# Optimization experiments

Hardware: AMD Instinct MI355X
Metric: run time of the kernel (lower is better)

## Reference

```python
import jax, jax.numpy as jnp
import numpy as np
import math

D = 384; N = 1024; BATCH = 8
D_STATE = 64; D_CONV = 4; EXPAND = 2
D_INNER = EXPAND * D
DT_RANK = math.ceil(D / 16)
W_WIN = 4; N_HEADS = 4; HEAD_DIM = D // N_HEADS
BOTTLENECK = max(8, D // 4)

def _perms(n):
    side = int(math.isqrt(n))
    p0 = np.arange(n)
    p1 = np.arange(n).reshape(side, side).T.reshape(-1)   # column-major
    p2 = p0[::-1].copy()                                   # reverse horizontal
    p3 = p1[::-1].copy()                                   # reverse vertical
    return [jnp.asarray(p) for p in (p0, p1, p2, p3)]

PERMS = _perms(N)

def layernorm(x, w, b, eps=1e-5):
    mu = jnp.mean(x, -1, keepdims=True)
    var = jnp.var(x, -1, keepdims=True)
    return (x - mu) * jax.lax.rsqrt(var + eps) * w + b

def mamba(x, in_proj_w, conv_w, conv_b, x_proj_w, dt_proj_w, dt_proj_b, A_log, D_skip, out_proj_w):
    # canonical pure-python Mamba block (selective scan SSM)
    B, L, _ = x.shape
    xz = x @ in_proj_w.T                      # [B,L,2*di]
    xin, z = jnp.split(xz, 2, axis=-1)
    xc = jnp.swapaxes(xin, 1, 2)              # [B,di,L]
    xc = jax.lax.conv_general_dilated(xc, conv_w, (1,), [(D_CONV - 1, 0)], feature_group_count=D_INNER)
    u = jax.nn.silu(jnp.swapaxes(xc + conv_b[None, :, None], 1, 2))  # [B,L,di]
    x_dbl = u @ x_proj_w.T                    # [B,L,dt_rank+2*ds]
    dt, Bm, Cm = jnp.split(x_dbl, [DT_RANK, DT_RANK + D_STATE], axis=-1)
    dt = jax.nn.softplus(dt @ dt_proj_w.T + dt_proj_b)  # [B,L,di]
    A = -jnp.exp(A_log)                       # [di,ds]
    def step(h, inp):
        dt_t, B_t, C_t, u_t = inp             # [B,di],[B,ds],[B,ds],[B,di]
        dA = jnp.exp(dt_t[:, :, None] * A[None])
        h = dA * h + dt_t[:, :, None] * B_t[:, None, :] * u_t[:, :, None]
        y = jnp.einsum('bds,bs->bd', h, C_t)
        return h, y
    h0 = jnp.zeros((B, D_INNER, D_STATE), x.dtype)
    xs = (jnp.swapaxes(dt, 0, 1), jnp.swapaxes(Bm, 0, 1), jnp.swapaxes(Cm, 0, 1), jnp.swapaxes(u, 0, 1))
    _, ys = jax.lax.scan(step, h0, xs)
    y = jnp.swapaxes(ys, 0, 1) + u * D_skip
    return (y * jax.nn.silu(z)) @ out_proj_w.T

def local_attn(x, qkv_w, qkv_b, ao_w, ao_b):
    # sliding-window MHA over windows of W_WIN tokens (N % W_WIN == 0 here, no pad)
    B, Nn, Dd = x.shape
    xw = x.reshape(B * (Nn // W_WIN), W_WIN, Dd)
    qkv = xw @ qkv_w.T + qkv_b
    q, k, v = jnp.split(qkv, 3, axis=-1)
    def heads(t):
        return t.reshape(t.shape[0], W_WIN, N_HEADS, HEAD_DIM).transpose(0, 2, 1, 3)
    q, k, v = heads(q), heads(k), heads(v)
    scores = jnp.einsum('bhqd,bhkd->bhqk', q, k) / math.sqrt(HEAD_DIM)
    attn = jax.nn.softmax(scores, axis=-1)
    o = jnp.einsum('bhqk,bhkd->bhqd', attn, v).transpose(0, 2, 1, 3).reshape(-1, W_WIN, Dd)
    return (o @ ao_w.T + ao_b).reshape(B, Nn, Dd)

def setup_inputs() -> dict:
    key = jax.random.key(0)
    ks = jax.random.split(key, 16)
    def rn(k, shape, scale=0.02):
        return jax.random.normal(k, shape, jnp.float32) * scale
    return dict(
        x=jax.random.normal(ks[0], (BATCH, N, D), jnp.float32),
        r_w1=rn(ks[1], (BOTTLENECK, D)), r_b1=jnp.zeros((BOTTLENECK,), jnp.float32),
        r_w2=rn(ks[2], (4, BOTTLENECK)), r_b2=jnp.zeros((4,), jnp.float32),
        ln1_w=jnp.ones((D,), jnp.float32), ln1_b=jnp.zeros((D,), jnp.float32),
        ln2_w=jnp.ones((D,), jnp.float32), ln2_b=jnp.zeros((D,), jnp.float32),
        in_proj_w=rn(ks[3], (2 * D_INNER, D)),
        conv_w=rn(ks[4], (D_INNER, 1, D_CONV), 0.1), conv_b=jnp.zeros((D_INNER,), jnp.float32),
        x_proj_w=rn(ks[5], (DT_RANK + 2 * D_STATE, D_INNER)),
        dt_proj_w=rn(ks[6], (D_INNER, DT_RANK), 0.1),
        dt_proj_b=jnp.full((D_INNER,), -3.0, jnp.float32) + rn(ks[7], (D_INNER,), 0.1),
        A_log=jnp.log(jnp.tile(jnp.arange(1, D_STATE + 1, dtype=jnp.float32), (D_INNER, 1))),
        D_skip=jnp.ones((D_INNER,), jnp.float32),
        out_proj_w=rn(ks[8], (D, D_INNER)),
        qkv_w=rn(ks[9], (3 * D, D)), qkv_b=jnp.zeros((3 * D,), jnp.float32),
        ao_w=rn(ks[10], (D, D)), ao_b=jnp.zeros((D,), jnp.float32),
        gate=jnp.full((1,), 0.1, jnp.float32),
        lng_w=jnp.ones((D,), jnp.float32), lng_b=jnp.zeros((D,), jnp.float32),
    )

def reference(x, r_w1, r_b1, r_w2, r_b2, ln1_w, ln1_b, ln2_w, ln2_b,
              in_proj_w, conv_w, conv_b, x_proj_w, dt_proj_w, dt_proj_b,
              A_log, D_skip, out_proj_w, qkv_w, qkv_b, ao_w, ao_b,
              gate, lng_w, lng_b):
    # ScanRouter: mean-pool -> MLP -> softmax over 4 directions (dropout=eval)
    g = jnp.mean(x, axis=1)
    h = jax.nn.gelu(g @ r_w1.T + r_b1, approximate=False)
    w = jax.nn.softmax(h @ r_w2.T + r_b2, axis=-1)   # [B,4]
    xn = layernorm(x, ln1_w, ln1_b)
    fused = jnp.zeros_like(x)
    for d in range(4):
        out = mamba(xn[:, PERMS[d], :], in_proj_w, conv_w, conv_b, x_proj_w,
                    dt_proj_w, dt_proj_b, A_log, D_skip, out_proj_w)
        fused = fused + w[:, d, None, None] * out
    x = x + fused                                    # residual (dropout=eval)
    xn2 = layernorm(x, ln2_w, ln2_b)
    ao = local_attn(xn2, qkv_w, qkv_b, ao_w, ao_b)
    return layernorm(xn2 + gate * ao, lng_w, lng_b)
```

## Files before the change

### kernel.cpp

```cpp
#include <hip/hip_runtime.h>
#include <math.h>


#define NSEQ  1024
#define DMODEL 384
#define DINNER 768
#define DSTATE 64
#define XW 152
#define SCHUNK 128

typedef unsigned short u16;
typedef __attribute__((ext_vector_type(8))) short short8;
typedef __attribute__((ext_vector_type(4))) float f32x4;

__device__ __forceinline__ float bf2f(u16 u){
  union { unsigned int i; float f; } c; c.i = ((unsigned int)u) << 16; return c.f;
}
__device__ __forceinline__ u16 f2bf(float f){
  union { float f; unsigned int i; } c; c.f = f;
  unsigned int x = c.i;
  return (u16)((x + 0x7fffu + ((x >> 16) & 1u)) >> 16);
}
__device__ __forceinline__ float4 unp4(uint2 u){
  float4 f;
  f.x = bf2f((u16)(u.x & 0xffffu)); f.y = bf2f((u16)(u.x >> 16));
  f.z = bf2f((u16)(u.y & 0xffffu)); f.w = bf2f((u16)(u.y >> 16));
  return f;
}

template<int DIR>
__device__ __forceinline__ int permi(int i){
  if (DIR == 0) return i;
  if (DIR == 1) return ((i & 31) << 5) | (i >> 5);
  if (DIR == 2) return 1023 - i;
  int j = 1023 - i; return ((j & 31) << 5) | (j >> 5);
}
template<int DIR>
__device__ __forceinline__ int znext(int zi){
  if (DIR == 0) return zi + 4;
  if (DIR == 2) return zi - 4;
  if (DIR == 1) { int t = zi + 128; return (t >= 1024) ? t - 1023 : t; }
  int t = zi - 128; return (t < 0) ? t + 1023 : t;
}

__global__ __launch_bounds__(384) void router_mean_kernel(const float* __restrict__ X, float* __restrict__ G){
  int b = blockIdx.y, chunk = blockIdx.x, c = threadIdx.x;
  float s = 0.f;
  const float* xp = X + ((size_t)b*NSEQ + (size_t)chunk*64)*DMODEL + c;
  for (int l = 0; l < 64; ++l) s += xp[(size_t)l*DMODEL];
  atomicAdd(&G[b*DMODEL + c], s * (1.f/1024.f));
}

__global__ __launch_bounds__(96) void router_mlp_kernel(const float* __restrict__ G,
    const float* __restrict__ w1, const float* __restrict__ b1,
    const float* __restrict__ w2, const float* __restrict__ b2, float* __restrict__ WR){
  int b = blockIdx.x, j = threadIdx.x;
  __shared__ float hs[96];
  __shared__ float ls[4];
  float a = b1[j];
  const float* g = G + b*DMODEL;
  for (int c = 0; c < DMODEL; ++c) a += g[c] * w1[j*DMODEL + c];
  hs[j] = 0.5f * a * (1.f + erff(a * 0.70710678118654752f));
  __syncthreads();
  if (j < 4) {
    float lg = b2[j];
    for (int jj = 0; jj < 96; ++jj) lg += hs[jj] * w2[j*96 + jj];
    ls[j] = lg;
  }
  __syncthreads();
  if (j == 0) {
    float mx = fmaxf(fmaxf(ls[0],ls[1]),fmaxf(ls[2],ls[3]));
    float e0=__expf(ls[0]-mx), e1=__expf(ls[1]-mx), e2=__expf(ls[2]-mx), e3=__expf(ls[3]-mx);
    float s = e0+e1+e2+e3;
    WR[b*4+0]=e0/s; WR[b*4+1]=e1/s; WR[b*4+2]=e2/s; WR[b*4+3]=e3/s;
  }
}

__global__ __launch_bounds__(256) void ln_bf16out_kernel(const float* __restrict__ X,
    const float* __restrict__ w, const float* __restrict__ bb, u16* __restrict__ O){
  int row = blockIdx.x*4 + (threadIdx.x >> 6);
  int lane = threadIdx.x & 63;
  const float* xr = X + (size_t)row*DMODEL;
  float v[6]; float s=0.f, s2=0.f;
  #pragma unroll
  for (int j=0;j<6;++j){ float t = xr[lane + j*64]; v[j]=t; s+=t; s2+=t*t; }
  #pragma unroll
  for (int m=1;m<64;m<<=1){ s += __shfl_xor(s,m,64); s2 += __shfl_xor(s2,m,64); }
  float mu = s*(1.f/DMODEL);
  float rs = rsqrtf(s2*(1.f/DMODEL) - mu*mu + 1e-5f);
  u16* o = O + (size_t)row*DMODEL;
  #pragma unroll
  for (int j=0;j<6;++j){ int i = lane+j*64; o[i] = f2bf((v[j]-mu)*rs*w[i] + bb[i]); }
}

__global__ __launch_bounds__(256) void ln_dual_kernel(const float* __restrict__ X,
    const float* __restrict__ w, const float* __restrict__ bb,
    float* __restrict__ O, u16* __restrict__ OB){
  int row = blockIdx.x*4 + (threadIdx.x >> 6);
  int lane = threadIdx.x & 63;
  const float* xr = X + (size_t)row*DMODEL;
  float v[6]; float s=0.f, s2=0.f;
  #pragma unroll
  for (int j=0;j<6;++j){ float t = xr[lane + j*64]; v[j]=t; s+=t; s2+=t*t; }
  #pragma unroll
  for (int m=1;m<64;m<<=1){ s += __shfl_xor(s,m,64); s2 += __shfl_xor(s2,m,64); }
  float mu = s*(1.f/DMODEL);
  float rs = rsqrtf(s2*(1.f/DMODEL) - mu*mu + 1e-5f);
  float* o = O + (size_t)row*DMODEL;
  u16* ob = OB + (size_t)row*DMODEL;
  #pragma unroll
  for (int j=0;j<6;++j){ int i = lane+j*64; float r = (v[j]-mu)*rs*w[i] + bb[i]; o[i] = r; ob[i] = f2bf(r); }
}

__global__ __launch_bounds__(256) void ln_final_kernel(const float* __restrict__ XN2,
    const float* __restrict__ AO, const float* __restrict__ gatep,
    const float* __restrict__ w, const float* __restrict__ bb, float* __restrict__ OUT){
  int row = blockIdx.x*4 + (threadIdx.x >> 6);
  int lane = threadIdx.x & 63;
  float gate = gatep[0];
  const float* xr = XN2 + (size_t)row*DMODEL;
  const float* ar = AO + (size_t)row*DMODEL;
  float v[6]; float s=0.f, s2=0.f;
  #pragma unroll
  for (int j=0;j<6;++j){ int i = lane+j*64; float t = xr[i] + gate*ar[i]; v[j]=t; s+=t; s2+=t*t; }
  #pragma unroll
  for (int m=1;m<64;m<<=1){ s += __shfl_xor(s,m,64); s2 += __shfl_xor(s2,m,64); }
  float mu = s*(1.f/DMODEL);
  float rs = rsqrtf(s2*(1.f/DMODEL) - mu*mu + 1e-5f);
  float* o = OUT + (size_t)row*DMODEL;
  #pragma unroll
  for (int j=0;j<6;++j){ int i = lane+j*64; o[i] = (v[j]-mu)*rs*w[i] + bb[i]; }
}

__global__ __launch_bounds__(256) void cvt4_kernel(const float* __restrict__ src,
    u16* __restrict__ dst, int n4){
  int i = blockIdx.x*256 + threadIdx.x;
  if (i >= n4) return;
  float4 v = ((const float4*)src)[i];
  ushort4 o; o.x=f2bf(v.x); o.y=f2bf(v.y); o.z=f2bf(v.z); o.w=f2bf(v.w);
  ((ushort4*)dst)[i] = o;
}

__global__ __launch_bounds__(256) void mgemm_kernel(
    const u16* __restrict__ A, int lda,
    const u16* __restrict__ W, int K, int N,
    const float* __restrict__ bias,
    const float* __restrict__ resid,
    int act,
    int obf,
    void* __restrict__ C, int ldc)
{
  const int lane = threadIdx.x & 63;
  const int wv = threadIdx.x >> 6;
  const int m0 = (blockIdx.y*4 + wv) * 64;
  const int n0 = blockIdx.x * 64;
  const int r  = lane & 15;
  const int kg = lane >> 4;
  f32x4 acc[4][4];
  #pragma unroll
  for (int i=0;i<4;++i){
    #pragma unroll
    for (int j=0;j<4;++j) acc[i][j] = (f32x4)0.f;
  }
  for (int k0 = 0; k0 < K; k0 += 32) {
    const bool kval = (k0 + kg*8) < K;
    short8 a[4], b[4];
    #pragma unroll
    for (int i = 0; i < 4; ++i) {
      a[i] = kval ? *(const short8*)(A + (size_t)(m0 + i*16 + r)*lda + k0 + kg*8) : (short8)0;
      int n = n0 + i*16 + r;
      b[i] = (kval && n < N) ? *(const short8*)(W + (size_t)n*K + k0 + kg*8) : (short8)0;
    }
    #pragma unroll
    for (int ai = 0; ai < 4; ++ai)
      #pragma unroll
      for (int bi = 0; bi < 4; ++bi)
        acc[ai][bi] = __builtin_amdgcn_mfma_f32_16x16x32_bf16(a[ai], b[bi], acc[ai][bi], 0, 0, 0);
  }
  #pragma unroll
  for (int ai = 0; ai < 4; ++ai) {
    int mrow = m0 + ai*16 + kg*4;
    #pragma unroll
    for (int bi = 0; bi < 4; ++bi) {
      int n = n0 + bi*16 + r;
      if (n < N) {
        #pragma unroll
        for (int q = 0; q < 4; ++q) {
          float v = acc[ai][bi][q];
          int m = mrow + q;
          if (bias) v += bias[n];
          if (act == 1) v = (v > 20.f) ? v : log1pf(__expf(v));
          if (resid) v += resid[(size_t)m*ldc + n];
          if (obf) ((u16*)C)[(size_t)m*ldc + n] = f2bf(v);
          else     ((float*)C)[(size_t)m*ldc + n] = v;
        }
      }
    }
  }
}

__global__ __launch_bounds__(256) void zsilu_kernel(u16* __restrict__ XZ){
  int idx = blockIdx.x*256 + threadIdx.x;
  int row = idx / 96, q = idx % 96;
  u16* p = XZ + (size_t)row*1536 + DINNER + q*8;
  uint4 v = *(uint4*)p;
  unsigned w0=v.x, w1=v.y, w2=v.z, w3=v.w;
  #define ZS(w) { \
    float lo = bf2f((u16)((w) & 0xffffu)); \
    float hi = bf2f((u16)((w) >> 16)); \
    lo = lo / (1.f + __expf(-lo)); \
    hi = hi / (1.f + __expf(-hi)); \
    (w) = (unsigned)f2bf(lo) | ((unsigned)f2bf(hi) << 16); }
  ZS(w0) ZS(w1) ZS(w2) ZS(w3)
  #undef ZS
  v.x=w0; v.y=w1; v.z=w2; v.w=w3;
  *(uint4*)p = v;
}

template<int DIR>
__device__ __forceinline__ float conv_acc(const u16* __restrict__ XZ,
    const float* __restrict__ cw, int b, int i, int c, float acc){
  #pragma unroll
  for (int k = 0; k < 4; ++k) {
    int ii = i - 3 + k;
    if (ii >= 0)
      acc += cw[c*4 + k] * bf2f(XZ[((size_t)b*NSEQ + permi<DIR>(ii))*1536 + c]);
  }
  return acc;
}

__global__ __launch_bounds__(256) void conv_silu_all_kernel(const u16* __restrict__ XZ,
    const float* __restrict__ cw, const float* __restrict__ cb,
    u16* __restrict__ UD4, int BS){
  int dir = blockIdx.y;
  int idx = blockIdx.x*256 + threadIdx.x;
  int c = idx % DINNER;
  int rest = idx / DINNER;
  int i = rest & 1023;
  int b = rest >> 10;
  float acc = cb[c];
  switch (dir) {
    case 0: acc = conv_acc<0>(XZ, cw, b, i, c, acc); break;
    case 1: acc = conv_acc<1>(XZ, cw, b, i, c, acc); break;
    case 2: acc = conv_acc<2>(XZ, cw, b, i, c, acc); break;
    default: acc = conv_acc<3>(XZ, cw, b, i, c, acc); break;
  }
  UD4[((size_t)(dir*BS + b)*NSEQ + i)*1536 + c] = f2bf(acc / (1.f + __expf(-acc)));
}

template<int CTRL>
__device__ __forceinline__ float dpp_add(float v){
  int t = __builtin_amdgcn_update_dpp(0, __float_as_int(v), CTRL, 0xf, 0xf, true);
  return v + __int_as_float(t);
}
__device__ __forceinline__ float row16_sum(float p){
  p = dpp_add<0x128>(p);
  p = dpp_add<0x124>(p);
  p = dpp_add<0x122>(p);
  p = dpp_add<0x121>(p);
  return p;
}

template<int DIR>
__device__ __forceinline__ void scan_body(
    const u16* __restrict__ xd, const u16* __restrict__ ud,
    const u16* __restrict__ zb,
    u16* __restrict__ ob,
    float* __restrict__ lacc,
    const float* __restrict__ A_log, const float* __restrict__ Dskip,
    float wgt, int c0w, int grp)
{
  const int lane = threadIdx.x & 63;
  const int g = lane >> 4;
  const int q = lane & 15;
  const int c = c0w + g;
  const float4 Alq = *(const float4*)(A_log + (size_t)c*DSTATE + q*4);
  const float As0 = -__expf(Alq.x), As1 = -__expf(Alq.y);
  const float As2 = -__expf(Alq.z), As3 = -__expf(Alq.w);
  const float dsk = Dskip[c];
  const u16* zp = zb + DINNER + c;
  float* lw = lacc + DIR*SCHUNK*8 + grp*4 + g;

  const u16* px0 = xd + 0*XW + 24 + q*4;
  const u16* px1 = xd + 1*XW + 24 + q*4;
  const u16* px2 = xd + 2*XW + 24 + q*4;
  const u16* px3 = xd + 3*XW + 24 + q*4;
  const u16* pu0 = ud + 0*1536 + c;
  const u16* pu1 = ud + 1*1536 + c;
  const u16* pu2 = ud + 2*1536 + c;
  const u16* pu3 = ud + 3*1536 + c;
  int zi0 = permi<DIR>(0), zi1 = permi<DIR>(1), zi2 = permi<DIR>(2), zi3 = permi<DIR>(3);

#define SLOAD(k) {                                                          \
    uint2 bd = *(const uint2*)px##k;                                        \
    uint2 cd = *(const uint2*)(px##k + 64);                                 \
    B##k = unp4(bd); C##k = unp4(cd);                                       \
    u##k = bf2f(pu##k[0]); t##k = bf2f(pu##k[768]);                         \
    z##k = bf2f(zp[(ptrdiff_t)zi##k * 1536]);                               \
    px##k += 4*XW; pu##k += 4*1536; zi##k = znext<DIR>(zi##k); }

#define SSTEP(k, l) {                                                       \
    float dtu = t##k * u##k;                                                \
    float e0 = __expf(t##k*As0), e1 = __expf(t##k*As1);                     \
    float e2 = __expf(t##k*As2), e3 = __expf(t##k*As3);                     \
    h0 = e0*h0 + dtu*B##k.x; h1 = e1*h1 + dtu*B##k.y;                       \
    h2 = e2*h2 + dtu*B##k.z; h3 = e3*h3 + dtu*B##k.w;                       \
    float p = h0*C##k.x + h1*C##k.y + h2*C##k.z + h3*C##k.w;                \
    p = row16_sum(p);                                                       \
    float o = wgt*(p + u##k*dsk)*z##k;                                      \
    if (q == 0) lw[((l)&(SCHUNK-1))*8] = o; }

  float4 B0,C0,B1,C1,B2,C2,B3,C3;
  float t0,u0,z0, t1,u1,z1, t2,u2,z2, t3,u3,z3;
  float h0=0.f, h1=0.f, h2=0.f, h3=0.f;
  SLOAD(0) SLOAD(1) SLOAD(2) SLOAD(3)
  __builtin_amdgcn_sched_barrier(0);
  for (int l0 = 0; l0 < NSEQ; l0 += SCHUNK) {
    for (int l = l0; l < l0 + SCHUNK; l += 4) {
      SSTEP(0,l)   SLOAD(0) __builtin_amdgcn_sched_barrier(0);
      SSTEP(1,l+1) SLOAD(1) __builtin_amdgcn_sched_barrier(0);
      SSTEP(2,l+2) SLOAD(2) __builtin_amdgcn_sched_barrier(0);
      SSTEP(3,l+3) SLOAD(3) __builtin_amdgcn_sched_barrier(0);
    }
    __syncthreads();
    for (int i = threadIdx.x; i < SCHUNK*8; i += 512) {
      float s = lacc[i] + lacc[SCHUNK*8 + i] + lacc[2*SCHUNK*8 + i] + lacc[3*SCHUNK*8 + i];
      int row = i >> 3, cc = i & 7;
      ob[(size_t)(l0 + row)*DINNER + cc] = f2bf(s);
    }
    __syncthreads();
  }
#undef SLOAD
#undef SSTEP
}

__global__ __launch_bounds__(512) void scan_all_kernel(
    const u16* __restrict__ XD4, const u16* __restrict__ UD4,
    const u16* __restrict__ XZ, u16* __restrict__ OB,
    const float* __restrict__ A_log, const float* __restrict__ Dskip,
    const float* __restrict__ WR, int b0, int BS)
{
  __shared__ float lacc[4*SCHUNK*8];
  const int bx = blockIdx.x;
  const int sx = (bx & 7)*12 + (bx >> 3);
  const int c0 = sx * 8;
  const int b = blockIdx.y;
  const int w = threadIdx.x >> 6;
  const int dir = w & 3;
  const int grp = w >> 2;
  const int c0w = c0 + grp*4;
  const size_t drb = ((size_t)dir*BS + b) * NSEQ;
  const u16* xd = XD4 + drb*XW;
  const u16* ud = UD4 + drb*1536;
  const u16* zz = XZ  + (size_t)b*NSEQ*1536;
  u16* ob = OB + (size_t)b*NSEQ*DINNER + c0;
  const float wgt = WR[(b0+b)*4 + dir];
  switch (dir) {
    case 0: scan_body<0>(xd, ud, zz, ob, lacc, A_log, Dskip, wgt, c0w, grp); break;
    case 1: scan_body<1>(xd, ud, zz, ob, lacc, A_log, Dskip, wgt, c0w, grp); break;
    case 2: scan_body<2>(xd, ud, zz, ob, lacc, A_log, Dskip, wgt, c0w, grp); break;
    default: scan_body<3>(xd, ud, zz, ob, lacc, A_log, Dskip, wgt, c0w, grp); break;
  }
}

__global__ __launch_bounds__(256) void attn_kernel(const float* __restrict__ QKV, u16* __restrict__ O){
  int idx = blockIdx.x*256 + threadIdx.x;
  int tq = idx & 3, h = (idx >> 2) & 3, w = idx >> 4;
  size_t row0 = (size_t)w * 4;
  const float4* qp = (const float4*)(QKV + (row0 + tq)*1152 + h*96);
  float sc[4];
  #pragma unroll
  for (int tk = 0; tk < 4; ++tk) {
    const float4* kp = (const float4*)(QKV + (row0 + tk)*1152 + 384 + h*96);
    float d = 0.f;
    #pragma unroll
    for (int j = 0; j < 24; ++j) {
      float4 qf = qp[j], kf = kp[j];
      d += qf.x*kf.x + qf.y*kf.y + qf.z*kf.z + qf.w*kf.w;
    }
    sc[tk] = d * 0.10206207261596575f;
  }
  float mx = fmaxf(fmaxf(sc[0],sc[1]),fmaxf(sc[2],sc[3]));
  float s = 0.f;
  #pragma unroll
  for (int tk=0;tk<4;++tk){ sc[tk]=__expf(sc[tk]-mx); s+=sc[tk]; }
  float inv = 1.f/s;
  #pragma unroll
  for (int tk=0;tk<4;++tk) sc[tk]*=inv;
  u16* op = O + (row0 + tq)*DMODEL + h*96;
  #pragma unroll 4
  for (int j = 0; j < 24; ++j) {
    float4 o = {0.f,0.f,0.f,0.f};
    #pragma unroll
    for (int tk=0;tk<4;++tk){
      const float4* vp = (const float4*)(QKV + (row0+tk)*1152 + 768 + h*96);
      float4 vf = vp[j];
      o.x += sc[tk]*vf.x; o.y += sc[tk]*vf.y; o.z += sc[tk]*vf.z; o.w += sc[tk]*vf.w;
    }
    ushort4 ov; ov.x=f2bf(o.x); ov.y=f2bf(o.y); ov.z=f2bf(o.z); ov.w=f2bf(o.w);
    *(ushort4*)(op + j*4) = ov;
  }
}

extern "C" void kernel_launch(void* const* d_in, const int* in_sizes, int n_in,
                              void* d_out, int out_size, void* d_ws, size_t ws_size,
                              hipStream_t stream)
{
  (void)in_sizes; (void)n_in; (void)out_size;
  const float* x         = (const float*)d_in[0];
  const float* r_w1      = (const float*)d_in[1];
  const float* r_b1      = (const float*)d_in[2];
  const float* r_w2      = (const float*)d_in[3];
  const float* r_b2      = (const float*)d_in[4];
  const float* ln1_w     = (const float*)d_in[5];
  const float* ln1_b     = (const float*)d_in[6];
  const float* ln2_w     = (const float*)d_in[7];
  const float* ln2_b     = (const float*)d_in[8];
  const float* in_proj_w = (const float*)d_in[9];
  const float* conv_w    = (const float*)d_in[10];
  const float* conv_b    = (const float*)d_in[11];
  const float* x_proj_w  = (const float*)d_in[12];
  const float* dt_proj_w = (const float*)d_in[13];
  const float* dt_proj_b = (const float*)d_in[14];
  const float* A_log     = (const float*)d_in[15];
  const float* D_skip    = (const float*)d_in[16];
  const float* out_proj_w= (const float*)d_in[17];
  const float* qkv_w     = (const float*)d_in[18];
  const float* qkv_b     = (const float*)d_in[19];
  const float* ao_w      = (const float*)d_in[20];
  const float* ao_b      = (const float*)d_in[21];
  const float* gate      = (const float*)d_in[22];
  const float* lng_w     = (const float*)d_in[23];
  const float* lng_b     = (const float*)d_in[24];

  float* ws = (float*)d_ws;
  float* WR = ws;
  float* G  = ws + 64;
  u16*  WBF = (u16*)(ws + 3200);
  u16* ipw = WBF + 0;
  u16* xpw = WBF + 589824;
  u16* dtw = WBF + 706560;
  u16* opw = WBF + 724992;
  u16* qkw = WBF + 1019904;
  u16* aow = WBF + 1462272;

  int BS = 8;
  while (BS > 1) {
    size_t need = ((size_t)808064 + (size_t)BS*1024*5296) * sizeof(float);
    if (need <= ws_size) break;
    BS >>= 1;
  }
  const int R = BS * 1024;

  (void)hipMemsetAsync(ws, 0, 4096*sizeof(float), stream);
  router_mean_kernel<<<dim3(16,8),384,0,stream>>>(x, G);
  router_mlp_kernel<<<8,96,0,stream>>>(G, r_w1, r_b1, r_w2, r_b2, WR);

  cvt4_kernel<<<576,256,0,stream>>>(in_proj_w, ipw, 147456);
  cvt4_kernel<<<114,256,0,stream>>>(x_proj_w,  xpw, 29184);
  cvt4_kernel<<<18,256,0,stream>>>(dt_proj_w,  dtw, 4608);
  cvt4_kernel<<<288,256,0,stream>>>(out_proj_w,opw, 73728);
  cvt4_kernel<<<432,256,0,stream>>>(qkv_w,     qkw, 110592);
  cvt4_kernel<<<144,256,0,stream>>>(ao_w,      aow, 36864);

  float* base = ws + 808064;
  u16*   ABF  = (u16*)base;
  u16*   XZbf = (u16*)(base + (size_t)R*384);
  u16*   UD4  = (u16*)(base + (size_t)R*1152);
  u16*   XD4  = (u16*)(base + (size_t)R*4224);
  float* XN2  = base + (size_t)R*4528;
  float* AOb  = base + (size_t)R*4912;
  float* X2   = (float*)UD4;
  float* QKV  = (float*)UD4 + (size_t)R*384;
  u16*   ATTO = (u16*)((float*)UD4 + (size_t)R*1536);

  for (int s = 0; s < 8/BS; ++s) {
    const int b0 = s * BS;
    const size_t xoff = (size_t)b0 * NSEQ * DMODEL;

    ln_bf16out_kernel<<<R/4,256,0,stream>>>(x + xoff, ln1_w, ln1_b, ABF);
    mgemm_kernel<<<dim3(24,R/256),256,0,stream>>>(ABF,384, ipw,384,1536, nullptr,nullptr,0,1, XZbf,1536);
    zsilu_kernel<<<(R*96)/256,256,0,stream>>>(XZbf);
    conv_silu_all_kernel<<<dim3(3*R,4),256,0,stream>>>(XZbf, conv_w, conv_b, UD4, BS);
    mgemm_kernel<<<dim3(3,R/64),256,0,stream>>>(UD4,1536, xpw,768,152, nullptr,nullptr,0,1, XD4,152);
    mgemm_kernel<<<dim3(12,R/64),256,0,stream>>>(XD4,152, dtw,24,768, dt_proj_b,nullptr,1,1, UD4+768,1536);
    scan_all_kernel<<<dim3(96,BS),512,0,stream>>>(XD4, UD4, XZbf, ABF, A_log, D_skip, WR, b0, BS);
    mgemm_kernel<<<dim3(6,R/256),256,0,stream>>>(ABF,768, opw,768,384, nullptr,x + xoff,0,0, X2,384);
    ln_dual_kernel<<<R/4,256,0,stream>>>(X2, ln2_w, ln2_b, XN2, ABF);
    mgemm_kernel<<<dim3(18,R/256),256,0,stream>>>(ABF,384, qkw,384,1152, qkv_b,nullptr,0,0, QKV,1152);
    attn_kernel<<<R/64,256,0,stream>>>(QKV, ATTO);
    mgemm_kernel<<<dim3(6,R/256),256,0,stream>>>(ATTO,384, aow,384,384, ao_b,nullptr,0,0, AOb,384);
    ln_final_kernel<<<R/4,256,0,stream>>>(XN2, AOb, gate, lng_w, lng_b, (float*)d_out + xoff);
  }
}
```

Baseline: 1.089 ms.

## Fuse z-SiLU into in_proj GEMM, fp32 x_proj output, scalar dt_proj, exp2 scan

Folds the SiLU on the z half into the in_proj GEMM epilogue and drops the separate zsilu pass. x_proj now writes fp32 instead of bf16. The dt projection becomes a plain scalar kernel that reads the fp32 x_proj output and the fp32 weights, replacing a MFMA GEMM with K=24. The scan uses raw v_exp_f32 with log2e folded into A, loads B/C as float4, and buffers four outputs so it issues one vector LDS store, using a transposed lacc layout. This trades more memory traffic for the fp32 intermediate and a scalar dt_proj against fewer launches and cheaper scan instructions.

```diff
diff --git a/kernel.cpp b/kernel.cpp
--- a/kernel.cpp
+++ b/kernel.cpp
@@ -21,11 +21,10 @@
   unsigned int x = c.i;
   return (u16)((x + 0x7fffu + ((x >> 16) & 1u)) >> 16);
 }
-__device__ __forceinline__ float4 unp4(uint2 u){
-  float4 f;
-  f.x = bf2f((u16)(u.x & 0xffffu)); f.y = bf2f((u16)(u.x >> 16));
-  f.z = bf2f((u16)(u.y & 0xffffu)); f.w = bf2f((u16)(u.y >> 16));
-  return f;
+__device__ __forceinline__ float exp2raw(float x){
+  float r;
+  asm("v_exp_f32 %0, %1" : "=v"(r) : "v"(x));
+  return r;
 }
 
 template<int DIR>
@@ -146,8 +145,7 @@
     const u16* __restrict__ W, int K, int N,
     const float* __restrict__ bias,
     const float* __restrict__ resid,
-    int act,
-    int obf,
+    int act, int obf,
     void* __restrict__ C, int ldc)
 {
   const int lane = threadIdx.x & 63;
@@ -190,6 +188,7 @@
           int m = mrow + q;
           if (bias) v += bias[n];
           if (act == 1) v = (v > 20.f) ? v : log1pf(__expf(v));
+          if (act == 2 && n >= DINNER) v = v / (1.f + __expf(-v));
           if (resid) v += resid[(size_t)m*ldc + n];
           if (obf) ((u16*)C)[(size_t)m*ldc + n] = f2bf(v);
           else     ((float*)C)[(size_t)m*ldc + n] = v;
@@ -199,22 +198,18 @@
   }
 }
 
-__global__ __launch_bounds__(256) void zsilu_kernel(u16* __restrict__ XZ){
+__global__ __launch_bounds__(256) void dtproj_kernel(const float* __restrict__ XDf,
+    const float* __restrict__ w, const float* __restrict__ b, u16* __restrict__ DT){
   int idx = blockIdx.x*256 + threadIdx.x;
-  int row = idx / 96, q = idx % 96;
-  u16* p = XZ + (size_t)row*1536 + DINNER + q*8;
-  uint4 v = *(uint4*)p;
-  unsigned w0=v.x, w1=v.y, w2=v.z, w3=v.w;
-  #define ZS(w) { \
-    float lo = bf2f((u16)((w) & 0xffffu)); \
-    float hi = bf2f((u16)((w) >> 16)); \
-    lo = lo / (1.f + __expf(-lo)); \
-    hi = hi / (1.f + __expf(-hi)); \
-    (w) = (unsigned)f2bf(lo) | ((unsigned)f2bf(hi) << 16); }
-  ZS(w0) ZS(w1) ZS(w2) ZS(w3)
-  #undef ZS
-  v.x=w0; v.y=w1; v.z=w2; v.w=w3;
-  *(uint4*)p = v;
+  int c = idx % DINNER;
+  int row = idx / DINNER;
+  const float* xr = XDf + (size_t)row*XW;
+  const float* wr = w + c*24;
+  float a = b[c];
+  #pragma unroll
+  for (int k = 0; k < 24; ++k) a += xr[k]*wr[k];
+  a = (a > 20.f) ? a : log1pf(__expf(a));
+  DT[(size_t)row*1536 + c] = f2bf(a);
 }
 
 template<int DIR>
@@ -263,7 +258,7 @@
 
 template<int DIR>
 __device__ __forceinline__ void scan_body(
-    const u16* __restrict__ xd, const u16* __restrict__ ud,
+    const float* __restrict__ xdf, const u16* __restrict__ ud,
     const u16* __restrict__ zb,
     u16* __restrict__ ob,
     float* __restrict__ lacc,
@@ -274,17 +269,18 @@
   const int g = lane >> 4;
   const int q = lane & 15;
   const int c = c0w + g;
+  const float L2E = 1.4426950408889634f;
   const float4 Alq = *(const float4*)(A_log + (size_t)c*DSTATE + q*4);
-  const float As0 = -__expf(Alq.x), As1 = -__expf(Alq.y);
-  const float As2 = -__expf(Alq.z), As3 = -__expf(Alq.w);
+  const float As0 = -__expf(Alq.x)*L2E, As1 = -__expf(Alq.y)*L2E;
+  const float As2 = -__expf(Alq.z)*L2E, As3 = -__expf(Alq.w)*L2E;
   const float dsk = Dskip[c];
   const u16* zp = zb + DINNER + c;
-  float* lw = lacc + DIR*SCHUNK*8 + grp*4 + g;
-
-  const u16* px0 = xd + 0*XW + 24 + q*4;
-  const u16* px1 = xd + 1*XW + 24 + q*4;
-  const u16* px2 = xd + 2*XW + 24 + q*4;
-  const u16* px3 = xd + 3*XW + 24 + q*4;
+  float* lw = lacc + DIR*(8*SCHUNK) + (grp*4 + g)*SCHUNK;
+
+  const float* px0 = xdf + 0*XW + 24 + q*4;
+  const float* px1 = xdf + 1*XW + 24 + q*4;
+  const float* px2 = xdf + 2*XW + 24 + q*4;
+  const float* px3 = xdf + 3*XW + 24 + q*4;
   const u16* pu0 = ud + 0*1536 + c;
   const u16* pu1 = ud + 1*1536 + c;
   const u16* pu2 = ud + 2*1536 + c;
@@ -292,23 +288,21 @@
   int zi0 = permi<DIR>(0), zi1 = permi<DIR>(1), zi2 = permi<DIR>(2), zi3 = permi<DIR>(3);
 
 #define SLOAD(k) {                                                          \
-    uint2 bd = *(const uint2*)px##k;                                        \
-    uint2 cd = *(const uint2*)(px##k + 64);                                 \
-    B##k = unp4(bd); C##k = unp4(cd);                                       \
+    B##k = *(const float4*)px##k;                                           \
+    C##k = *(const float4*)(px##k + 64);                                    \
     u##k = bf2f(pu##k[0]); t##k = bf2f(pu##k[768]);                         \
     z##k = bf2f(zp[(ptrdiff_t)zi##k * 1536]);                               \
     px##k += 4*XW; pu##k += 4*1536; zi##k = znext<DIR>(zi##k); }
 
-#define SSTEP(k, l) {                                                       \
+#define SSTEP(k, ov_) {                                                     \
     float dtu = t##k * u##k;                                                \
-    float e0 = __expf(t##k*As0), e1 = __expf(t##k*As1);                     \
-    float e2 = __expf(t##k*As2), e3 = __expf(t##k*As3);                     \
+    float e0 = exp2raw(t##k*As0), e1 = exp2raw(t##k*As1);                   \
+    float e2 = exp2raw(t##k*As2), e3 = exp2raw(t##k*As3);                   \
     h0 = e0*h0 + dtu*B##k.x; h1 = e1*h1 + dtu*B##k.y;                       \
     h2 = e2*h2 + dtu*B##k.z; h3 = e3*h3 + dtu*B##k.w;                       \
     float p = h0*C##k.x + h1*C##k.y + h2*C##k.z + h3*C##k.w;                \
     p = row16_sum(p);                                                       \
-    float o = wgt*(p + u##k*dsk)*z##k;                                      \
-    if (q == 0) lw[((l)&(SCHUNK-1))*8] = o; }
+    ov_ = wgt*(p + u##k*dsk)*z##k; }
 
   float4 B0,C0,B1,C1,B2,C2,B3,C3;
   float t0,u0,z0, t1,u1,z1, t2,u2,z2, t3,u3,z3;
@@ -317,15 +311,22 @@
   __builtin_amdgcn_sched_barrier(0);
   for (int l0 = 0; l0 < NSEQ; l0 += SCHUNK) {
     for (int l = l0; l < l0 + SCHUNK; l += 4) {
-      SSTEP(0,l)   SLOAD(0) __builtin_amdgcn_sched_barrier(0);
-      SSTEP(1,l+1) SLOAD(1) __builtin_amdgcn_sched_barrier(0);
-      SSTEP(2,l+2) SLOAD(2) __builtin_amdgcn_sched_barrier(0);
-      SSTEP(3,l+3) SLOAD(3) __builtin_amdgcn_sched_barrier(0);
+      float o0,o1,o2,o3;
+      SSTEP(0,o0) SLOAD(0) __builtin_amdgcn_sched_barrier(0);
+      SSTEP(1,o1) SLOAD(1) __builtin_amdgcn_sched_barrier(0);
+      SSTEP(2,o2) SLOAD(2) __builtin_amdgcn_sched_barrier(0);
+      SSTEP(3,o3) SLOAD(3)
+      if (q == 0) {
+        float4 ov = {o0,o1,o2,o3};
+        *(float4*)(lw + (l & (SCHUNK-1))) = ov;
+      }
+      __builtin_amdgcn_sched_barrier(0);
     }
     __syncthreads();
-    for (int i = threadIdx.x; i < SCHUNK*8; i += 512) {
-      float s = lacc[i] + lacc[SCHUNK*8 + i] + lacc[2*SCHUNK*8 + i] + lacc[3*SCHUNK*8 + i];
-      int row = i >> 3, cc = i & 7;
+    for (int i = threadIdx.x; i < 8*SCHUNK; i += 512) {
+      int cc = i & 7, row = i >> 3;
+      int li = cc*SCHUNK + row;
+      float s = lacc[li] + lacc[8*SCHUNK + li] + lacc[16*SCHUNK + li] + lacc[24*SCHUNK + li];
       ob[(size_t)(l0 + row)*DINNER + cc] = f2bf(s);
     }
     __syncthreads();
@@ -335,12 +336,12 @@
 }
 
 __global__ __launch_bounds__(512) void scan_all_kernel(
-    const u16* __restrict__ XD4, const u16* __restrict__ UD4,
+    const float* __restrict__ XD4f, const u16* __restrict__ UD4,
     const u16* __restrict__ XZ, u16* __restrict__ OB,
     const float* __restrict__ A_log, const float* __restrict__ Dskip,
     const float* __restrict__ WR, int b0, int BS)
 {
-  __shared__ float lacc[4*SCHUNK*8];
+  __shared__ float lacc[4*8*SCHUNK];
   const int bx = blockIdx.x;
   const int sx = (bx & 7)*12 + (bx >> 3);
   const int c0 = sx * 8;
@@ -350,16 +351,16 @@
   const int grp = w >> 2;
   const int c0w = c0 + grp*4;
   const size_t drb = ((size_t)dir*BS + b) * NSEQ;
-  const u16* xd = XD4 + drb*XW;
+  const float* xdf = XD4f + drb*XW;
   const u16* ud = UD4 + drb*1536;
   const u16* zz = XZ  + (size_t)b*NSEQ*1536;
   u16* ob = OB + (size_t)b*NSEQ*DINNER + c0;
   const float wgt = WR[(b0+b)*4 + dir];
   switch (dir) {
-    case 0: scan_body<0>(xd, ud, zz, ob, lacc, A_log, Dskip, wgt, c0w, grp); break;
-    case 1: scan_body<1>(xd, ud, zz, ob, lacc, A_log, Dskip, wgt, c0w, grp); break;
-    case 2: scan_body<2>(xd, ud, zz, ob, lacc, A_log, Dskip, wgt, c0w, grp); break;
-    default: scan_body<3>(xd, ud, zz, ob, lacc, A_log, Dskip, wgt, c0w, grp); break;
+    case 0: scan_body<0>(xdf, ud, zz, ob, lacc, A_log, Dskip, wgt, c0w, grp); break;
+    case 1: scan_body<1>(xdf, ud, zz, ob, lacc, A_log, Dskip, wgt, c0w, grp); break;
+    case 2: scan_body<2>(xdf, ud, zz, ob, lacc, A_log, Dskip, wgt, c0w, grp); break;
+    default: scan_body<3>(xdf, ud, zz, ob, lacc, A_log, Dskip, wgt, c0w, grp); break;
   }
 }
 
@@ -439,14 +440,13 @@
   u16*  WBF = (u16*)(ws + 3200);
   u16* ipw = WBF + 0;
   u16* xpw = WBF + 589824;
-  u16* dtw = WBF + 706560;
   u16* opw = WBF + 724992;
   u16* qkw = WBF + 1019904;
   u16* aow = WBF + 1462272;
 
   int BS = 8;
   while (BS > 1) {
-    size_t need = ((size_t)808064 + (size_t)BS*1024*5296) * sizeof(float);
+    size_t need = ((size_t)808064 + (size_t)BS*1024*5600) * sizeof(float);
     if (need <= ws_size) break;
     BS >>= 1;
   }
@@ -458,7 +458,6 @@
 
   cvt4_kernel<<<576,256,0,stream>>>(in_proj_w, ipw, 147456);
   cvt4_kernel<<<114,256,0,stream>>>(x_proj_w,  xpw, 29184);
-  cvt4_kernel<<<18,256,0,stream>>>(dt_proj_w,  dtw, 4608);
   cvt4_kernel<<<288,256,0,stream>>>(out_proj_w,opw, 73728);
   cvt4_kernel<<<432,256,0,stream>>>(qkv_w,     qkw, 110592);
   cvt4_kernel<<<144,256,0,stream>>>(ao_w,      aow, 36864);
@@ -467,9 +466,9 @@
   u16*   ABF  = (u16*)base;
   u16*   XZbf = (u16*)(base + (size_t)R*384);
   u16*   UD4  = (u16*)(base + (size_t)R*1152);
-  u16*   XD4  = (u16*)(base + (size_t)R*4224);
-  float* XN2  = base + (size_t)R*4528;
-  float* AOb  = base + (size_t)R*4912;
+  float* XD4f = base + (size_t)R*4224;
+  float* XN2  = base + (size_t)R*4832;
+  float* AOb  = base + (size_t)R*5216;
   float* X2   = (float*)UD4;
   float* QKV  = (float*)UD4 + (size_t)R*384;
   u16*   ATTO = (u16*)((float*)UD4 + (size_t)R*1536);
@@ -479,12 +478,11 @@
     const size_t xoff = (size_t)b0 * NSEQ * DMODEL;
 
     ln_bf16out_kernel<<<R/4,256,0,stream>>>(x + xoff, ln1_w, ln1_b, ABF);
-    mgemm_kernel<<<dim3(24,R/256),256,0,stream>>>(ABF,384, ipw,384,1536, nullptr,nullptr,0,1, XZbf,1536);
-    zsilu_kernel<<<(R*96)/256,256,0,stream>>>(XZbf);
+    mgemm_kernel<<<dim3(24,R/256),256,0,stream>>>(ABF,384, ipw,384,1536, nullptr,nullptr,2,1, XZbf,1536);
     conv_silu_all_kernel<<<dim3(3*R,4),256,0,stream>>>(XZbf, conv_w, conv_b, UD4, BS);
-    mgemm_kernel<<<dim3(3,R/64),256,0,stream>>>(UD4,1536, xpw,768,152, nullptr,nullptr,0,1, XD4,152);
-    mgemm_kernel<<<dim3(12,R/64),256,0,stream>>>(XD4,152, dtw,24,768, dt_proj_b,nullptr,1,1, UD4+768,1536);
-    scan_all_kernel<<<dim3(96,BS),512,0,stream>>>(XD4, UD4, XZbf, ABF, A_log, D_skip, WR, b0, BS);
+    mgemm_kernel<<<dim3(3,R/64),256,0,stream>>>(UD4,1536, xpw,768,152, nullptr,nullptr,0,0, XD4f,152);
+    dtproj_kernel<<<12*R,256,0,stream>>>(XD4f, dt_proj_w, dt_proj_b, UD4+768);
+    scan_all_kernel<<<dim3(96,BS),512,0,stream>>>(XD4f, UD4, XZbf, ABF, A_log, D_skip, WR, b0, BS);
     mgemm_kernel<<<dim3(6,R/256),256,0,stream>>>(ABF,768, opw,768,384, nullptr,x + xoff,0,0, X2,384);
     ln_dual_kernel<<<R/4,256,0,stream>>>(X2, ln2_w, ln2_b, XN2, ABF);
     mgemm_kernel<<<dim3(18,R/256),256,0,stream>>>(ABF,384, qkw,384,1152, qkv_b,nullptr,0,0, QKV,1152);
```

Result: slower. 1.188 ms (+9.1%).
